# Optimization experiments

Measured on AMD Instinct MI355X. Metric: run time of the kernel, lower is better.

The kernel has to match this reference:

```python
import jax, jax.numpy as jnp
import numpy as np

NUM_NODES = 50000
DIM = 64
NUM_LAYERS = 2
NUM_EDGES = 800000
EPS = 1e-12


def _l2_normalize(x):
    # F.normalize(x, dim=1): x / max(||x||_2, eps)
    n = jnp.sqrt(jnp.sum(x * x, axis=1, keepdims=True))
    return x / jnp.maximum(n, EPS)


def _lgconv(x, src, dst):
    # PyG LGConv: symmetric gcn_norm without self-loops.
    # deg computed at target nodes; out[dst] += d^-1/2[src] * d^-1/2[dst] * x[src]
    ones = jnp.ones(src.shape[0], dtype=x.dtype)
    deg = jax.ops.segment_sum(ones, dst, num_segments=NUM_NODES)
    dinv = jnp.where(deg > 0, 1.0 / jnp.sqrt(jnp.where(deg > 0, deg, 1.0)), 0.0)
    norm = dinv[src] * dinv[dst]  # [E]
    msg = norm[:, None] * x[src]  # [E, D] gather + scale
    return jax.ops.segment_sum(msg, dst, num_segments=NUM_NODES)


def _propagate(x, edge_index):
    src, dst = edge_index[0], edge_index[1]
    for _ in range(NUM_LAYERS):
        x = _lgconv(x, src, dst)
    return _l2_normalize(x)


def setup_inputs() -> dict:
    key = jax.random.key(0)
    k1, k2, k3, k4 = jax.random.split(key, 4)
    x = jax.random.normal(k1, (NUM_NODES, DIM), dtype=jnp.float32)
    alpha = jnp.ones((3,), dtype=jnp.float32)
    ei_t = jax.random.randint(k2, (2, NUM_EDGES), 0, NUM_NODES, dtype=jnp.int32)
    ei_y = jax.random.randint(k3, (2, NUM_EDGES), 0, NUM_NODES, dtype=jnp.int32)
    ei_c = jax.random.randint(k4, (2, NUM_EDGES), 0, NUM_NODES, dtype=jnp.int32)
    return {"x": x, "alpha": alpha, "edge_index_title": ei_t,
            "edge_index_year": ei_y, "edge_index_cat": ei_c}


def reference(x, alpha, edge_index_title, edge_index_year, edge_index_cat):
    x = _l2_normalize(x)
    x_title = _propagate(x, edge_index_title)
    x_year = _propagate(x, edge_index_year)
    x_cat = _propagate(x, edge_index_cat)
    w = jax.nn.softmax(alpha, axis=0)
    w = jnp.clip(w, 0.0001, None)
    w = w / jnp.sum(w)
    return w[0] * x_title + w[1] * x_year + w[2] * x_cat
```

## Files before the change

### kernel.cpp

```cpp
#include <hip/hip_runtime.h>
#include <hip/hip_bf16.h>

#define NUM_NODES 50000
#define DIM 64
#define NUM_EDGES 800000
#define NUM_GRAPHS 3
#define TOT_NODES (NUM_NODES * NUM_GRAPHS)
#define EPS 1e-12f

#define NB2 391
#define TB2 (NB2 * NUM_GRAPHS)
#define PCAP2 2816
#define P3_CHUNK 4096
#define P3_BLOCKS ((NUM_EDGES + P3_CHUNK - 1) / P3_CHUNK)

typedef unsigned short ushort_t;
typedef unsigned int uint_t;
typedef unsigned int uint4v __attribute__((ext_vector_type(4)));
typedef unsigned short ushort8v __attribute__((ext_vector_type(8)));
typedef float f32x8 __attribute__((ext_vector_type(8)));

__device__ __forceinline__ ushort_t f2bf(float f) {
    uint_t x = __float_as_uint(f);
    uint_t r = (x + 0x7FFFu + ((x >> 16) & 1u)) >> 16;
    return (ushort_t)r;
}

__device__ __forceinline__ f32x8 unpack8(uint4v w) {
    f32x8 r;
    r[0] = __uint_as_float(w[0] << 16);
    r[1] = __uint_as_float(w[0] & 0xFFFF0000u);
    r[2] = __uint_as_float(w[1] << 16);
    r[3] = __uint_as_float(w[1] & 0xFFFF0000u);
    r[4] = __uint_as_float(w[2] << 16);
    r[5] = __uint_as_float(w[2] & 0xFFFF0000u);
    r[6] = __uint_as_float(w[3] << 16);
    r[7] = __uint_as_float(w[3] & 0xFFFF0000u);
    return r;
}

__global__ void l2norm_kernel(const float* __restrict__ in, ushort_t* __restrict__ out) {
    int row = blockIdx.x * (blockDim.x >> 6) + (threadIdx.x >> 6);
    int lane = threadIdx.x & 63;
    if (row >= NUM_NODES) return;
    float v = in[(long)row * DIM + lane];
    float s = v * v;
    #pragma unroll
    for (int off = 32; off > 0; off >>= 1)
        s += __shfl_xor(s, off, 64);
    float inv = 1.0f / fmaxf(sqrtf(s), EPS);
    out[(long)row * DIM + lane] = f2bf(v * inv);
}

__global__ __launch_bounds__(512) void partition_kernel(
        const int* __restrict__ e0, const int* __restrict__ e1, const int* __restrict__ e2,
        int* __restrict__ gcnt, uint_t* __restrict__ part) {
    __shared__ uint_t recs[P3_CHUNK];
    __shared__ int h[NB2], lstart[NB2], gbase[NB2], lcur[NB2];
    __shared__ int wsum[8];

    int g = blockIdx.y;
    const int* ei = (g == 0) ? e0 : (g == 1) ? e1 : e2;
    const int* srcp = ei;
    const int* dstp = ei + NUM_EDGES;
    int base = blockIdx.x * P3_CHUNK;
    int n = min(P3_CHUNK, NUM_EDGES - base);
    int t = threadIdx.x;
    int wid = t >> 6, ln = t & 63;

    for (int i = t; i < NB2; i += 512) h[i] = 0;
    __syncthreads();
    for (int i = t; i < n; i += 512)
        atomicAdd(&h[dstp[base + i] >> 7], 1);
    __syncthreads();

    {
        int v = (t < NB2) ? h[t] : 0;
        int s = v;
        #pragma unroll
        for (int off = 1; off < 64; off <<= 1) {
            int u = __shfl_up(s, off, 64);
            if (ln >= off) s += u;
        }
        if (ln == 63) wsum[wid] = s;
        __syncthreads();
        int prefix = 0;
        #pragma unroll
        for (int w = 0; w < 8; ++w)
            if (w < wid) prefix += wsum[w];
        if (t < NB2) {
            int ex = prefix + s - v;
            lstart[t] = ex;
            lcur[t] = ex;
            gbase[t] = (v > 0) ? atomicAdd(&gcnt[g * NB2 + t], v) : 0;
        }
    }
    __syncthreads();

    for (int i = t; i < n; i += 512) {
        int s = srcp[base + i];
        int d = dstp[base + i];
        int pos = atomicAdd(&lcur[d >> 7], 1);
        recs[pos] = ((uint_t)d << 16) | (uint_t)s;
    }
    __syncthreads();

    for (int i = t; i < n; i += 512) {
        uint_t r = recs[i];
        int b = r >> 23;
        int off = gbase[b] + (i - lstart[b]);
        if (off < PCAP2)
            part[(long)(g * NB2 + b) * PCAP2 + off] = r;
    }
}

__global__ __launch_bounds__(512) void bucket_sort_kernel(
        uint_t* __restrict__ part, const int* __restrict__ gcnt,
        int* __restrict__ row_start, int* __restrict__ row_end, float* __restrict__ dinv) {
    __shared__ uint_t recs[PCAP2];
    __shared__ ushort_t es_l[PCAP2];
    __shared__ int hist[128], lcur[128];
    __shared__ int w0sum;

    int b = blockIdx.x;
    int g = b / NB2;
    int bhi = b - g * NB2;
    long s0 = (long)b * PCAP2;
    int n = min(gcnt[b], PCAP2);
    int t = threadIdx.x;
    int ln = t & 63;

    if (t < 128) hist[t] = 0;
    __syncthreads();
    for (int i = t; i < n; i += 512) {
        uint_t r = part[s0 + i];
        recs[i] = r;
        atomicAdd(&hist[(r >> 16) & 127], 1);
    }
    __syncthreads();

    int v = (t < 128) ? hist[t] : 0;
    int s = v;
    #pragma unroll
    for (int off = 1; off < 64; off <<= 1) {
        int u = __shfl_up(s, off, 64);
        if (ln >= off) s += u;
    }
    if (t == 63) w0sum = s;
    __syncthreads();
    if (t < 128) {
        int prefix = (t >= 64) ? w0sum : 0;
        int ex = prefix + s - v;
        lcur[t] = ex;
        int node = (bhi << 7) + t;
        if (node < NUM_NODES) {
            int k = g * NUM_NODES + node;
            int base = (int)(2 * s0);
            row_start[k] = base + ex;
            row_end[k]   = base + ex + v;
            dinv[k] = (v > 0) ? rsqrtf((float)v) : 0.0f;
        }
    }
    __syncthreads();

    for (int i = t; i < n; i += 512) {
        uint_t r = recs[i];
        int dl = (r >> 16) & 127;
        int pos = atomicAdd(&lcur[dl], 1);
        es_l[pos] = (ushort_t)(r & 0xFFFFu);
    }
    __syncthreads();
    uint_t* es_out = (uint_t*)((ushort_t*)part + 2 * s0);
    int nw = (n + 1) >> 1;
    const uint_t* es_lw = (const uint_t*)es_l;
    for (int i = t; i < nw; i += 512)
        es_out[i] = es_lw[i];
}

__global__ void conv1_all_kernel(const ushort_t* __restrict__ xn,
                                 const ushort_t* __restrict__ esort,
                                 const int* __restrict__ row_start,
                                 const int* __restrict__ row_end,
                                 const float* __restrict__ dinv,
                                 ushort_t* __restrict__ bufA) {
    int row = blockIdx.x * (blockDim.x >> 6) + (threadIdx.x >> 6);
    int g = blockIdx.y;
    int lane = threadIdx.x & 63;
    int sub = lane >> 3;
    int li  = lane & 7;
    if (row >= NUM_NODES) return;

    int k = g * NUM_NODES + row;
    int start = __builtin_amdgcn_readfirstlane(row_start[k]);
    int end   = __builtin_amdgcn_readfirstlane(row_end[k]);
    const float* dv = dinv + g * NUM_NODES;

    f32x8 a = {0, 0, 0, 0, 0, 0, 0, 0};

    int i = start;
    for (; i + 32 <= end; i += 32) {
        int s0 = esort[i + sub];
        int s1 = esort[i + 8 + sub];
        int s2 = esort[i + 16 + sub];
        int s3 = esort[i + 24 + sub];
        float d0 = dv[s0], d1 = dv[s1], d2 = dv[s2], d3 = dv[s3];
        uint4v w0 = *(const uint4v*)(xn + (long)s0 * DIM + li * 8);
        uint4v w1 = *(const uint4v*)(xn + (long)s1 * DIM + li * 8);
        uint4v w2 = *(const uint4v*)(xn + (long)s2 * DIM + li * 8);
        uint4v w3 = *(const uint4v*)(xn + (long)s3 * DIM + li * 8);
        a += unpack8(w0) * d0;
        a += unpack8(w1) * d1;
        a += unpack8(w2) * d2;
        a += unpack8(w3) * d3;
    }
    for (; i + 16 <= end; i += 16) {
        int s0 = esort[i + sub];
        int s1 = esort[i + 8 + sub];
        float d0 = dv[s0], d1 = dv[s1];
        uint4v w0 = *(const uint4v*)(xn + (long)s0 * DIM + li * 8);
        uint4v w1 = *(const uint4v*)(xn + (long)s1 * DIM + li * 8);
        a += unpack8(w0) * d0;
        a += unpack8(w1) * d1;
    }
    for (; i < end; i += 8) {
        int e = i + sub;
        if (e < end) {
            int s = esort[e];
            float d = dv[s];
            uint4v w = *(const uint4v*)(xn + (long)s * DIM + li * 8);
            a += unpack8(w) * d;
        }
    }
    #pragma unroll
    for (int off = 8; off < 64; off <<= 1) {
        #pragma unroll
        for (int j = 0; j < 8; ++j)
            a[j] += __shfl_xor(a[j], off, 64);
    }
    float dt = dv[row];
    float scl = dt * dt;
    if (sub == 0) {
        ushort8v o;
        #pragma unroll
        for (int j = 0; j < 8; ++j) o[j] = f2bf(a[j] * scl);
        *(ushort8v*)(bufA + (long)k * DIM + li * 8) = o;
    }
}

__global__ void conv2_finalize_kernel(const ushort_t* __restrict__ bufA,
                                      const ushort_t* __restrict__ esort,
                                      const int* __restrict__ row_start,
                                      const int* __restrict__ row_end,
                                      const float* __restrict__ alpha,
                                      float* __restrict__ out) {
    int row = blockIdx.x * (blockDim.x >> 6) + (threadIdx.x >> 6);
    int lane = threadIdx.x & 63;
    int sub = lane >> 3;
    int li  = lane & 7;
    if (row >= NUM_NODES) return;

    float al0 = alpha[0], al1 = alpha[1], al2 = alpha[2];
    float m = fmaxf(al0, fmaxf(al1, al2));
    float e0 = expf(al0 - m), e1 = expf(al1 - m), e2 = expf(al2 - m);
    float es = e0 + e1 + e2;
    float w0 = fmaxf(e0 / es, 1e-4f);
    float w1 = fmaxf(e1 / es, 1e-4f);
    float w2 = fmaxf(e2 / es, 1e-4f);
    float wsum = w0 + w1 + w2;

    f32x8 res = {0, 0, 0, 0, 0, 0, 0, 0};

    #pragma unroll
    for (int g = 0; g < NUM_GRAPHS; ++g) {
        int k = g * NUM_NODES + row;
        int start = __builtin_amdgcn_readfirstlane(row_start[k]);
        int end   = __builtin_amdgcn_readfirstlane(row_end[k]);
        const ushort_t* tbl = bufA + (long)g * NUM_NODES * DIM;

        f32x8 a = {0, 0, 0, 0, 0, 0, 0, 0};

        int i = start;
        for (; i + 32 <= end; i += 32) {
            int s0 = esort[i + sub];
            int s1 = esort[i + 8 + sub];
            int s2 = esort[i + 16 + sub];
            int s3 = esort[i + 24 + sub];
            uint4v v0 = *(const uint4v*)(tbl + (long)s0 * DIM + li * 8);
            uint4v v1 = *(const uint4v*)(tbl + (long)s1 * DIM + li * 8);
            uint4v v2 = *(const uint4v*)(tbl + (long)s2 * DIM + li * 8);
            uint4v v3 = *(const uint4v*)(tbl + (long)s3 * DIM + li * 8);
            a += unpack8(v0);
            a += unpack8(v1);
            a += unpack8(v2);
            a += unpack8(v3);
        }
        for (; i + 16 <= end; i += 16) {
            int s0 = esort[i + sub];
            int s1 = esort[i + 8 + sub];
            uint4v v0 = *(const uint4v*)(tbl + (long)s0 * DIM + li * 8);
            uint4v v1 = *(const uint4v*)(tbl + (long)s1 * DIM + li * 8);
            a += unpack8(v0);
            a += unpack8(v1);
        }
        for (; i < end; i += 8) {
            int e = i + sub;
            if (e < end) {
                int s = esort[e];
                uint4v w = *(const uint4v*)(tbl + (long)s * DIM + li * 8);
                a += unpack8(w);
            }
        }
        #pragma unroll
        for (int off = 8; off < 64; off <<= 1) {
            #pragma unroll
            for (int j = 0; j < 8; ++j)
                a[j] += __shfl_xor(a[j], off, 64);
        }
        float s = 0.0f;
        #pragma unroll
        for (int j = 0; j < 8; ++j) s += a[j] * a[j];
        #pragma unroll
        for (int off = 1; off < 8; off <<= 1)
            s += __shfl_xor(s, off, 64);
        float wg = ((g == 0) ? w0 : (g == 1) ? w1 : w2) / wsum;
        float scl = wg / fmaxf(sqrtf(s), EPS);
        res += a * scl;
    }

    if (sub == 0) {
        float* p = out + (long)row * DIM + li * 8;
        *(float4*)p = make_float4(res[0], res[1], res[2], res[3]);
        *(float4*)(p + 4) = make_float4(res[4], res[5], res[6], res[7]);
    }
}

extern "C" void kernel_launch(void* const* d_in, const int* in_sizes, int n_in,
                              void* d_out, int out_size, void* d_ws, size_t ws_size,
                              hipStream_t stream) {
    const float* x     = (const float*)d_in[0];
    const float* alpha = (const float*)d_in[1];
    const int* e0 = (const int*)d_in[2];
    const int* e1 = (const int*)d_in[3];
    const int* e2 = (const int*)d_in[4];
    float* out = (float*)d_out;

    ushort_t* xn   = (ushort_t*)d_ws;
    ushort_t* bufA = xn + (long)NUM_NODES * DIM;
    float* dinv    = (float*)(bufA + (long)TOT_NODES * DIM);
    int* row_start = (int*)(dinv + TOT_NODES);
    int* row_end   = row_start + 150016;
    int* gcnt      = row_end + 150016;
    uint_t* part   = (uint_t*)(gcnt + 1176);

    const int wave_grid = (NUM_NODES * 64 + 255) / 256;

    l2norm_kernel<<<wave_grid, 256, 0, stream>>>(x, xn);

    hipMemsetAsync(gcnt, 0, TB2 * sizeof(int), stream);
    {
        dim3 grd(P3_BLOCKS, NUM_GRAPHS);
        partition_kernel<<<grd, 512, 0, stream>>>(e0, e1, e2, gcnt, part);
    }
    bucket_sort_kernel<<<TB2, 512, 0, stream>>>(part, gcnt, row_start, row_end, dinv);

    const ushort_t* esort = (const ushort_t*)part;

    {
        dim3 grd(wave_grid, NUM_GRAPHS);
        conv1_all_kernel<<<grd, 256, 0, stream>>>(xn, esort, row_start, row_end, dinv, bufA);
    }
    conv2_finalize_kernel<<<wave_grid, 256, 0, stream>>>(bufA, esort, row_start, row_end, alpha, out);
}
```

Before: 237.1 us.

## Premultiply features by dinv per graph and process two rows per wave

The l2norm kernel now runs after the degree sort and writes three bf16 copies of the normalized features, each prescaled by that graph's dinv[src]. This removes the per-edge dinv gather from conv1. Both conv kernels now give half a wave (32 lanes, 4 edge slots) to each destination row, so short rows (about 16 edges on average) waste fewer lanes and the shuffle reduction is shorter. The cost is extra writes for the tripled feature buffer, and start/end are no longer wave-uniform, so the loops may diverge within a wave.

```diff
diff --git a/kernel.cpp b/kernel.cpp
--- a/kernel.cpp
+++ b/kernel.cpp
@@ -39,19 +39,6 @@
     return r;
 }
 
-__global__ void l2norm_kernel(const float* __restrict__ in, ushort_t* __restrict__ out) {
-    int row = blockIdx.x * (blockDim.x >> 6) + (threadIdx.x >> 6);
-    int lane = threadIdx.x & 63;
-    if (row >= NUM_NODES) return;
-    float v = in[(long)row * DIM + lane];
-    float s = v * v;
-    #pragma unroll
-    for (int off = 32; off > 0; off >>= 1)
-        s += __shfl_xor(s, off, 64);
-    float inv = 1.0f / fmaxf(sqrtf(s), EPS);
-    out[(long)row * DIM + lane] = f2bf(v * inv);
-}
-
 __global__ __launch_bounds__(512) void partition_kernel(
         const int* __restrict__ e0, const int* __restrict__ e1, const int* __restrict__ e2,
         int* __restrict__ gcnt, uint_t* __restrict__ part) {
@@ -177,67 +164,67 @@
         es_out[i] = es_lw[i];
 }
 
-__global__ void conv1_all_kernel(const ushort_t* __restrict__ xn,
-                                 const ushort_t* __restrict__ esort,
-                                 const int* __restrict__ row_start,
-                                 const int* __restrict__ row_end,
-                                 const float* __restrict__ dinv,
-                                 ushort_t* __restrict__ bufA) {
+__global__ void l2norm_premult_kernel(const float* __restrict__ x,
+                                      const float* __restrict__ dinv,
+                                      ushort_t* __restrict__ bufX) {
     int row = blockIdx.x * (blockDim.x >> 6) + (threadIdx.x >> 6);
+    int lane = threadIdx.x & 63;
+    if (row >= NUM_NODES) return;
+    float v = x[(long)row * DIM + lane];
+    float s = v * v;
+    #pragma unroll
+    for (int off = 32; off > 0; off >>= 1)
+        s += __shfl_xor(s, off, 64);
+    float nv = v / fmaxf(sqrtf(s), EPS);
+    #pragma unroll
+    for (int g = 0; g < NUM_GRAPHS; ++g) {
+        float d = dinv[g * NUM_NODES + row];
+        bufX[(long)(g * NUM_NODES + row) * DIM + lane] = f2bf(nv * d);
+    }
+}
+
+__global__ void conv1_kernel(const ushort_t* __restrict__ bufX,
+                             const ushort_t* __restrict__ esort,
+                             const int* __restrict__ row_start,
+                             const int* __restrict__ row_end,
+                             const float* __restrict__ dinv,
+                             ushort_t* __restrict__ bufA) {
+    int pair = blockIdx.x * (blockDim.x >> 6) + (threadIdx.x >> 6);
     int g = blockIdx.y;
     int lane = threadIdx.x & 63;
-    int sub = lane >> 3;
-    int li  = lane & 7;
+    int half = lane >> 5;
+    int sub  = (lane >> 3) & 3;
+    int li   = lane & 7;
+    int row = pair * 2 + half;
     if (row >= NUM_NODES) return;
 
     int k = g * NUM_NODES + row;
-    int start = __builtin_amdgcn_readfirstlane(row_start[k]);
-    int end   = __builtin_amdgcn_readfirstlane(row_end[k]);
-    const float* dv = dinv + g * NUM_NODES;
+    int start = row_start[k];
+    int end   = row_end[k];
+    const ushort_t* tbl = bufX + (long)g * NUM_NODES * DIM;
 
     f32x8 a = {0, 0, 0, 0, 0, 0, 0, 0};
-
-    int i = start;
-    for (; i + 32 <= end; i += 32) {
-        int s0 = esort[i + sub];
-        int s1 = esort[i + 8 + sub];
-        int s2 = esort[i + 16 + sub];
-        int s3 = esort[i + 24 + sub];
-        float d0 = dv[s0], d1 = dv[s1], d2 = dv[s2], d3 = dv[s3];
-        uint4v w0 = *(const uint4v*)(xn + (long)s0 * DIM + li * 8);
-        uint4v w1 = *(const uint4v*)(xn + (long)s1 * DIM + li * 8);
-        uint4v w2 = *(const uint4v*)(xn + (long)s2 * DIM + li * 8);
-        uint4v w3 = *(const uint4v*)(xn + (long)s3 * DIM + li * 8);
-        a += unpack8(w0) * d0;
-        a += unpack8(w1) * d1;
-        a += unpack8(w2) * d2;
-        a += unpack8(w3) * d3;
-    }
-    for (; i + 16 <= end; i += 16) {
-        int s0 = esort[i + sub];
-        int s1 = esort[i + 8 + sub];
-        float d0 = dv[s0], d1 = dv[s1];
-        uint4v w0 = *(const uint4v*)(xn + (long)s0 * DIM + li * 8);
-        uint4v w1 = *(const uint4v*)(xn + (long)s1 * DIM + li * 8);
-        a += unpack8(w0) * d0;
-        a += unpack8(w1) * d1;
-    }
-    for (; i < end; i += 8) {
-        int e = i + sub;
-        if (e < end) {
-            int s = esort[e];
-            float d = dv[s];
-            uint4v w = *(const uint4v*)(xn + (long)s * DIM + li * 8);
-            a += unpack8(w) * d;
-        }
-    }
-    #pragma unroll
-    for (int off = 8; off < 64; off <<= 1) {
+    int i = start + sub;
+    for (; i + 4 < end; i += 8) {
+        int s0 = esort[i];
+        int s1 = esort[i + 4];
+        uint4v w0 = *(const uint4v*)(tbl + (long)s0 * DIM + li * 8);
+        uint4v w1 = *(const uint4v*)(tbl + (long)s1 * DIM + li * 8);
+        a += unpack8(w0);
+        a += unpack8(w1);
+    }
+    if (i < end) {
+        int s = esort[i];
+        uint4v w = *(const uint4v*)(tbl + (long)s * DIM + li * 8);
+        a += unpack8(w);
+    }
+    #pragma unroll
+    for (int off = 8; off < 32; off <<= 1) {
         #pragma unroll
         for (int j = 0; j < 8; ++j)
             a[j] += __shfl_xor(a[j], off, 64);
     }
-    float dt = dv[row];
+    float dt = dinv[k];
     float scl = dt * dt;
     if (sub == 0) {
         ushort8v o;
@@ -253,10 +240,12 @@
                                       const int* __restrict__ row_end,
                                       const float* __restrict__ alpha,
                                       float* __restrict__ out) {
-    int row = blockIdx.x * (blockDim.x >> 6) + (threadIdx.x >> 6);
+    int pair = blockIdx.x * (blockDim.x >> 6) + (threadIdx.x >> 6);
     int lane = threadIdx.x & 63;
-    int sub = lane >> 3;
-    int li  = lane & 7;
+    int half = lane >> 5;
+    int sub  = (lane >> 3) & 3;
+    int li   = lane & 7;
+    int row = pair * 2 + half;
     if (row >= NUM_NODES) return;
 
     float al0 = alpha[0], al1 = alpha[1], al2 = alpha[2];
@@ -273,45 +262,27 @@
     #pragma unroll
     for (int g = 0; g < NUM_GRAPHS; ++g) {
         int k = g * NUM_NODES + row;
-        int start = __builtin_amdgcn_readfirstlane(row_start[k]);
-        int end   = __builtin_amdgcn_readfirstlane(row_end[k]);
+        int start = row_start[k];
+        int end   = row_end[k];
         const ushort_t* tbl = bufA + (long)g * NUM_NODES * DIM;
 
         f32x8 a = {0, 0, 0, 0, 0, 0, 0, 0};
-
-        int i = start;
-        for (; i + 32 <= end; i += 32) {
-            int s0 = esort[i + sub];
-            int s1 = esort[i + 8 + sub];
-            int s2 = esort[i + 16 + sub];
-            int s3 = esort[i + 24 + sub];
-            uint4v v0 = *(const uint4v*)(tbl + (long)s0 * DIM + li * 8);
-            uint4v v1 = *(const uint4v*)(tbl + (long)s1 * DIM + li * 8);
-            uint4v v2 = *(const uint4v*)(tbl + (long)s2 * DIM + li * 8);
-            uint4v v3 = *(const uint4v*)(tbl + (long)s3 * DIM + li * 8);
-            a += unpack8(v0);
-            a += unpack8(v1);
-            a += unpack8(v2);
-            a += unpack8(v3);
-        }
-        for (; i + 16 <= end; i += 16) {
-            int s0 = esort[i + sub];
-            int s1 = esort[i + 8 + sub];
+        int i = start + sub;
+        for (; i + 4 < end; i += 8) {
+            int s0 = esort[i];
+            int s1 = esort[i + 4];
             uint4v v0 = *(const uint4v*)(tbl + (long)s0 * DIM + li * 8);
             uint4v v1 = *(const uint4v*)(tbl + (long)s1 * DIM + li * 8);
             a += unpack8(v0);
             a += unpack8(v1);
         }
-        for (; i < end; i += 8) {
-            int e = i + sub;
-            if (e < end) {
-                int s = esort[e];
-                uint4v w = *(const uint4v*)(tbl + (long)s * DIM + li * 8);
-                a += unpack8(w);
-            }
-        }
-        #pragma unroll
-        for (int off = 8; off < 64; off <<= 1) {
+        if (i < end) {
+            int s = esort[i];
+            uint4v w = *(const uint4v*)(tbl + (long)s * DIM + li * 8);
+            a += unpack8(w);
+        }
+        #pragma unroll
+        for (int off = 8; off < 32; off <<= 1) {
             #pragma unroll
             for (int j = 0; j < 8; ++j)
                 a[j] += __shfl_xor(a[j], off, 64);
@@ -344,8 +315,8 @@
     const int* e2 = (const int*)d_in[4];
     float* out = (float*)d_out;
 
-    ushort_t* xn   = (ushort_t*)d_ws;
-    ushort_t* bufA = xn + (long)NUM_NODES * DIM;
+    ushort_t* bufX = (ushort_t*)d_ws;
+    ushort_t* bufA = bufX + (long)TOT_NODES * DIM;
     float* dinv    = (float*)(bufA + (long)TOT_NODES * DIM);
     int* row_start = (int*)(dinv + TOT_NODES);
     int* row_end   = row_start + 150016;
@@ -353,8 +324,7 @@
     uint_t* part   = (uint_t*)(gcnt + 1176);
 
     const int wave_grid = (NUM_NODES * 64 + 255) / 256;
-
-    l2norm_kernel<<<wave_grid, 256, 0, stream>>>(x, xn);
+    const int pair_grid = ((NUM_NODES / 2) * 64 + 255) / 256;
 
     hipMemsetAsync(gcnt, 0, TB2 * sizeof(int), stream);
     {
@@ -365,9 +335,11 @@
 
     const ushort_t* esort = (const ushort_t*)part;
 
+    l2norm_premult_kernel<<<wave_grid, 256, 0, stream>>>(x, dinv, bufX);
+
     {
-        dim3 grd(wave_grid, NUM_GRAPHS);
-        conv1_all_kernel<<<grd, 256, 0, stream>>>(xn, esort, row_start, row_end, dinv, bufA);
-    }
-    conv2_finalize_kernel<<<wave_grid, 256, 0, stream>>>(bufA, esort, row_start, row_end, alpha, out);
-}
+        dim3 grd(pair_grid, NUM_GRAPHS);
+        conv1_kernel<<<grd, 256, 0, stream>>>(bufX, esort, row_start, row_end, dinv, bufA);
+    }
+    conv2_finalize_kernel<<<pair_grid, 256, 0, stream>>>(bufA, esort, row_start, row_end, alpha, out);
+}
```

Result: faster. 209.2 us (-11.8%).
